# Kernel optimization log

Hardware: AMD Instinct MI355X
Metric: run time of the kernel (lower is better)

## Reference

```python
import jax, jax.numpy as jnp
import numpy as np

N = 50000          # num nodes
E = 800000         # num edges
NEG_SLOPE = 0.2    # leaky relu slope for attention logits


def gat_layer(h, W, al, ar, src, dst, res_W=None, res_identity=False, apply_elu=False):
    """One GATConv layer (DGL semantics, dropout=0, fc bias-free).
    h: [N, F_in]; W: [F_in, H*D]; al, ar: [H, D]. Returns [N, H, D]."""
    H, D = al.shape
    feat = (h @ W).reshape(N, H, D)                      # projected features
    el = jnp.sum(feat * al, axis=-1)                     # [N, H]
    er = jnp.sum(feat * ar, axis=-1)                     # [N, H]
    e = jax.nn.leaky_relu(el[src] + er[dst], NEG_SLOPE)  # [E, H] edge logits
    # numerically-stable edge softmax segmented over destination nodes
    m = jax.ops.segment_max(e, dst, num_segments=N)      # [N, H]
    m = jnp.where(jnp.isfinite(m), m, 0.0)               # nodes with no in-edges
    ex = jnp.exp(e - m[dst])
    den = jax.ops.segment_sum(ex, dst, num_segments=N)   # [N, H]
    alpha = ex / (den[dst] + 1e-9)                       # [E, H]
    # message passing: gather src feats, weight by alpha, scatter-add to dst
    out = jax.ops.segment_sum(feat[src] * alpha[..., None], dst, num_segments=N)
    if res_identity:
        out = out + h.reshape(N, H, D)
    elif res_W is not None:
        out = out + (h @ res_W).reshape(N, H, D)
    if apply_elu:
        out = jax.nn.elu(out)
    return out


def setup_inputs() -> dict:
    key = jax.random.key(0)
    ks = jax.random.split(key, 14)
    s = 0.1  # keep attention logits tame
    return {
        "features": jax.random.normal(ks[0], (N, 128), jnp.float32),
        "W0": jax.random.normal(ks[1], (128, 128), jnp.float32) * s,
        "al0": jax.random.normal(ks[2], (4, 32), jnp.float32) * s,
        "ar0": jax.random.normal(ks[3], (4, 32), jnp.float32) * s,
        "W1": jax.random.normal(ks[4], (128, 128), jnp.float32) * s,
        "al1": jax.random.normal(ks[5], (4, 32), jnp.float32) * s,
        "ar1": jax.random.normal(ks[6], (4, 32), jnp.float32) * s,
        "W2": jax.random.normal(ks[7], (128, 40), jnp.float32) * s,
        "al2": jax.random.normal(ks[8], (1, 40), jnp.float32) * s,
        "ar2": jax.random.normal(ks[9], (1, 40), jnp.float32) * s,
        "resW2": jax.random.normal(ks[10], (128, 40), jnp.float32) * s,
        "src": jax.random.randint(ks[11], (E,), 0, N, jnp.int32),
        "dst": jax.random.randint(ks[12], (E,), 0, N, jnp.int32),
    }


def reference(features, W0, al0, ar0, W1, al1, ar1, W2, al2, ar2, resW2, src, dst):
    # hidden layer 0: no residual, elu, flatten heads
    h = gat_layer(features, W0, al0, ar0, src, dst, apply_elu=True).reshape(N, -1)
    # hidden layer 1: residual (identity since in == heads*out), elu, flatten
    h = gat_layer(h, W1, al1, ar1, src, dst, res_identity=True, apply_elu=True).reshape(N, -1)
    # output layer: residual projection, no activation, mean over heads
    logits = gat_layer(h, W2, al2, ar2, src, dst, res_W=resW2).mean(axis=1)
    return logits
```

## Files before the change

kernel.cpp:

```cpp
#include <hip/hip_runtime.h>
#include <hip/hip_fp16.h>

#define NNODES 50000
#define NEDGES 800000

typedef _Float16 f16x8 __attribute__((ext_vector_type(8)));
typedef float f32x4 __attribute__((ext_vector_type(4)));

__global__ void k_count(const int* __restrict__ dst, int* __restrict__ cnt, int ne) {
  int e = blockIdx.x * 256 + threadIdx.x;
  if (e < ne) atomicAdd(&cnt[dst[e]], 1);
}

__global__ __launch_bounds__(1024) void k_blocksum(const int* __restrict__ cnt,
                                                   int* __restrict__ bsum, int n) {
  __shared__ int sb[1024];
  int t = threadIdx.x, i = blockIdx.x * 1024 + t;
  sb[t] = (i < n) ? cnt[i] : 0;
  __syncthreads();
  for (int m = 512; m; m >>= 1) {
    if (t < m) sb[t] += sb[t + m];
    __syncthreads();
  }
  if (t == 0) bsum[blockIdx.x] = sb[0];
}

__global__ void k_scanb(const int* __restrict__ bsum, int* __restrict__ bpre, int nb) {
  if (threadIdx.x == 0) {
    int s = 0;
    for (int i = 0; i < nb; ++i) { bpre[i] = s; s += bsum[i]; }
  }
}

__global__ __launch_bounds__(1024) void k_scanwrite(int* __restrict__ cnt,
                                                    const int* __restrict__ bpre,
                                                    int* __restrict__ row_off, int n) {
  __shared__ int sb[1024];
  int t = threadIdx.x, i = blockIdx.x * 1024 + t;
  int v = (i < n) ? cnt[i] : 0;
  sb[t] = v;
  __syncthreads();
  for (int off = 1; off < 1024; off <<= 1) {
    int x = (t >= off) ? sb[t - off] : 0;
    __syncthreads();
    sb[t] += x;
    __syncthreads();
  }
  int incl = sb[t] + bpre[blockIdx.x];
  if (i < n) {
    row_off[i + 1] = incl;
    cnt[i] = incl - v;
  }
  if (i == 0) row_off[0] = 0;
}

__global__ void k_fill(const int* __restrict__ src, const int* __restrict__ dst,
                       int* __restrict__ cursor, int* __restrict__ esrc, int ne) {
  int e = blockIdx.x * 256 + threadIdx.x;
  if (e < ne) {
    int pos = atomicAdd(&cursor[dst[e]], 1);
    esrc[pos] = src[e];
  }
}

__global__ __launch_bounds__(128) void k_prep(const float* __restrict__ W0, const float* __restrict__ al0,
                                              const float* __restrict__ ar0,
                                              const float* __restrict__ W1, const float* __restrict__ al1,
                                              const float* __restrict__ ar1,
                                              const float* __restrict__ W2, const float* __restrict__ resW2,
                                              const float* __restrict__ al2, const float* __restrict__ ar2,
                                              _Float16* __restrict__ Wt0, _Float16* __restrict__ Wt1,
                                              _Float16* __restrict__ Wt2) {
  int b = blockIdx.x, k = threadIdx.x;
  if (b < 288) {
    const float* W = (b < 144) ? W0 : W1;
    const float* al = (b < 144) ? al0 : al1;
    const float* ar = (b < 144) ? ar0 : ar1;
    _Float16* Wt = (b < 144) ? Wt0 : Wt1;
    int c = (b < 144) ? b : b - 144;
    float v = 0.f;
    if (c < 128) {
      v = W[k * 128 + c];
    } else if (c < 136) {
      int h = c - 128;
      const float* av = (h < 4) ? al : ar;
      int hh = h & 3;
      float s = 0.f;
      for (int d = 0; d < 32; ++d) s += W[k * 128 + hh * 32 + d] * av[hh * 32 + d];
      v = s;
    }
    Wt[c * 128 + k] = (_Float16)v;
  } else {
    int c = b - 288;
    float v = 0.f;
    if (c < 40) {
      v = W2[k * 40 + c];
    } else if (c < 80) {
      v = resW2[k * 40 + (c - 40)];
    } else if (c == 80) {
      float s = 0.f;
      for (int d = 0; d < 40; ++d) s += W2[k * 40 + d] * al2[d];
      v = s;
    } else if (c == 81) {
      float s = 0.f;
      for (int d = 0; d < 40; ++d) s += W2[k * 40 + d] * ar2[d];
      v = s;
    }
    Wt2[c * 128 + k] = (_Float16)v;
  }
}

template <int NCT, bool L2E>
__global__ __launch_bounds__(512) void k_gemm_mfma(const float* __restrict__ A,
                                                   const _Float16* __restrict__ Wtg,
                                                   __half* __restrict__ C,
                                                   float* __restrict__ resOut,
                                                   float* __restrict__ el,
                                                   float* __restrict__ er, int nrows) {
  __shared__ _Float16 Ah[128 * 136];
  __shared__ _Float16 Wl[NCT * 16 * 136];
  int t = threadIdx.x;
  int r0 = blockIdx.x * 128;

  for (int q = t; q < NCT * 16 * 16; q += 512) {
    int row = q >> 4, k8 = (q & 15) * 8;
    *(f16x8*)(&Wl[row * 136 + k8]) = *(const f16x8*)(Wtg + row * 128 + k8);
  }
  #pragma unroll
  for (int p = 0; p < 8; ++p) {
    int q = p * 512 + t;
    int r = q >> 5, k4 = (q & 31) * 4;
    float4 v = make_float4(0.f, 0.f, 0.f, 0.f);
    if (r0 + r < nrows) v = *(const float4*)(A + (size_t)(r0 + r) * 128 + k4);
    union { _Float16 h[4]; uint2 u; } pk;
    pk.h[0] = (_Float16)v.x; pk.h[1] = (_Float16)v.y;
    pk.h[2] = (_Float16)v.z; pk.h[3] = (_Float16)v.w;
    *(uint2*)(&Ah[r * 136 + k4]) = pk.u;
  }
  __syncthreads();

  int wave = t >> 6, l = t & 63;
  const _Float16* abase = &Ah[(wave * 16 + (l & 15)) * 136 + ((l >> 4) * 8)];
  const _Float16* bbase = &Wl[(l & 15) * 136 + ((l >> 4) * 8)];

  f32x4 acc[NCT] = {};
  #pragma unroll
  for (int ks = 0; ks < 4; ++ks) {
    f16x8 af = *(const f16x8*)(abase + ks * 32);
    #pragma unroll
    for (int nt = 0; nt < NCT; ++nt) {
      f16x8 bf = *(const f16x8*)(bbase + nt * 16 * 136 + ks * 32);
      acc[nt] = __builtin_amdgcn_mfma_f32_16x16x32_f16(af, bf, acc[nt], 0, 0, 0);
    }
  }

  int cc = l & 15;
  int rbase = r0 + wave * 16 + (l >> 4) * 4;
  #pragma unroll
  for (int r = 0; r < 4; ++r) {
    int row = rbase + r;
    if (row >= nrows) continue;
    if (!L2E) {
      #pragma unroll
      for (int nt = 0; nt < 8; ++nt)
        C[(size_t)row * 128 + nt * 16 + cc] = __float2half_rn(acc[nt][r]);
      float v = acc[8][r];
      if (cc < 4) el[row * 4 + cc] = v;
      else if (cc < 8) er[row * 4 + (cc - 4)] = v;
    } else {
      #pragma unroll
      for (int nt = 0; nt < 6; ++nt) {
        int col = nt * 16 + cc;
        float v = acc[nt][r];
        if (col < 40) C[(size_t)row * 40 + col] = __float2half_rn(v);
        else if (col < 80) resOut[(size_t)row * 40 + (col - 40)] = v;
        else if (col == 80) el[row] = v;
        else if (col == 81) er[row] = v;
      }
    }
  }
}

__device__ __forceinline__ void fma8h(float4& a0, float4& a1, float w, const uint4& r) {
  const __half2* hp = (const __half2*)&r;
  float2 f0 = __half22float2(hp[0]);
  float2 f1 = __half22float2(hp[1]);
  float2 f2 = __half22float2(hp[2]);
  float2 f3 = __half22float2(hp[3]);
  a0.x += w * f0.x; a0.y += w * f0.y; a0.z += w * f1.x; a0.w += w * f1.y;
  a1.x += w * f2.x; a1.y += w * f2.y; a1.z += w * f3.x; a1.w += w * f3.y;
}

template <bool RES, bool DOELU>
__global__ __launch_bounds__(256) void k_msg128v4(const __half* __restrict__ feat,
                                                  const float* __restrict__ el,
                                                  const float* __restrict__ er,
                                                  const int* __restrict__ row_off,
                                                  const int* __restrict__ esrc,
                                                  const float* __restrict__ hres,
                                                  float* __restrict__ out, int nnodes) {
  int t = threadIdx.x;
  int n = blockIdx.x * 16 + (t >> 4);
  if (n >= nnodes) return;
  int lane = t & 15;
  int h = lane >> 2;
  int s = row_off[n], e = row_off[n + 1];
  float ern = er[n * 4 + h];
  float4 acc0[4] = {}, acc1[4] = {};
  float den[4] = {0.f, 0.f, 0.f, 0.f};

  for (int c = s; c < e; c += 16) {
    int m = e - c; if (m > 16) m = 16;
    int sjv = 0;
    if (lane < m) sjv = esrc[c + lane];
    int e0 = __shfl(sjv, (lane & 3), 16);
    int e1 = __shfl(sjv, (lane & 3) + 4, 16);
    int e2 = __shfl(sjv, (lane & 3) + 8, 16);
    int e3 = __shfl(sjv, (lane & 3) + 12, 16);
    float sel0 = el[e0 * 4 + h];
    float sel1 = el[e1 * 4 + h];
    float sel2 = el[e2 * 4 + h];
    float sel3 = el[e3 * 4 + h];

#define GAT_SUB(KK, SEL)                                                      \
    {                                                                         \
      int b = KK * 4;                                                         \
      if (b < m) {                                                            \
        int mm = m - b; if (mm > 4) mm = 4;                                   \
        _Pragma("unroll")                                                     \
        for (int j = 0; j < 4; ++j) {                                         \
          if (j < mm) {                                                       \
            float ev = __shfl(SEL, (lane & 12) | j, 16);                      \
            float x = ev + ern;                                               \
            x = fmaxf(x, 0.2f * x);                                           \
            float wgt = __expf(x);                                            \
            int sj = __shfl(sjv, b + j, 16);                                  \
            den[j] += wgt;                                                    \
            uint4 raw = *(const uint4*)(feat + (size_t)sj * 128 + lane * 8);  \
            fma8h(acc0[j], acc1[j], wgt, raw);                                \
          }                                                                   \
        }                                                                     \
      }                                                                       \
    }
    GAT_SUB(0, sel0)
    GAT_SUB(1, sel1)
    GAT_SUB(2, sel2)
    GAT_SUB(3, sel3)
#undef GAT_SUB
  }

  float4 A0, A1;
  A0.x = (acc0[0].x + acc0[1].x) + (acc0[2].x + acc0[3].x);
  A0.y = (acc0[0].y + acc0[1].y) + (acc0[2].y + acc0[3].y);
  A0.z = (acc0[0].z + acc0[1].z) + (acc0[2].z + acc0[3].z);
  A0.w = (acc0[0].w + acc0[1].w) + (acc0[2].w + acc0[3].w);
  A1.x = (acc1[0].x + acc1[1].x) + (acc1[2].x + acc1[3].x);
  A1.y = (acc1[0].y + acc1[1].y) + (acc1[2].y + acc1[3].y);
  A1.z = (acc1[0].z + acc1[1].z) + (acc1[2].z + acc1[3].z);
  A1.w = (acc1[0].w + acc1[1].w) + (acc1[2].w + acc1[3].w);
  float D = (den[0] + den[1]) + (den[2] + den[3]);
  float inv = (e > s) ? 1.f / D : 0.f;
  A0.x *= inv; A0.y *= inv; A0.z *= inv; A0.w *= inv;
  A1.x *= inv; A1.y *= inv; A1.z *= inv; A1.w *= inv;
  if (RES) {
    float4 r0 = *(const float4*)(hres + (size_t)n * 128 + lane * 8);
    float4 r1 = *(const float4*)(hres + (size_t)n * 128 + lane * 8 + 4);
    A0.x += r0.x; A0.y += r0.y; A0.z += r0.z; A0.w += r0.w;
    A1.x += r1.x; A1.y += r1.y; A1.z += r1.z; A1.w += r1.w;
  }
  if (DOELU) {
    A0.x = (A0.x > 0.f) ? A0.x : expm1f(A0.x);
    A0.y = (A0.y > 0.f) ? A0.y : expm1f(A0.y);
    A0.z = (A0.z > 0.f) ? A0.z : expm1f(A0.z);
    A0.w = (A0.w > 0.f) ? A0.w : expm1f(A0.w);
    A1.x = (A1.x > 0.f) ? A1.x : expm1f(A1.x);
    A1.y = (A1.y > 0.f) ? A1.y : expm1f(A1.y);
    A1.z = (A1.z > 0.f) ? A1.z : expm1f(A1.z);
    A1.w = (A1.w > 0.f) ? A1.w : expm1f(A1.w);
  }
  *(float4*)(out + (size_t)n * 128 + lane * 8) = A0;
  *(float4*)(out + (size_t)n * 128 + lane * 8 + 4) = A1;
}

__global__ __launch_bounds__(256) void k_msg40v4(const __half* __restrict__ feat,
                                                 const float* __restrict__ el,
                                                 const float* __restrict__ er,
                                                 const int* __restrict__ row_off,
                                                 const int* __restrict__ esrc,
                                                 const float* __restrict__ res,
                                                 float* __restrict__ out, int nnodes) {
  int t = threadIdx.x;
  int n = blockIdx.x * 16 + (t >> 4);
  if (n >= nnodes) return;
  int lane = t & 15;
  int s = row_off[n], e = row_off[n + 1];
  float ern = er[n];
  float4 acc[2] = {};
  float den[2] = {0.f, 0.f};

  for (int c = s; c < e; c += 16) {
    int m = e - c; if (m > 16) m = 16;
    int sjv = 0;
    if (lane < m) sjv = esrc[c + lane];
    float selv = el[sjv];
    #pragma unroll
    for (int j = 0; j < 16; ++j) {
      if (j < m) {
        float ev = __shfl(selv, j, 16);
        float x = ev + ern;
        x = fmaxf(x, 0.2f * x);
        float wgt = __expf(x);
        int sj = __shfl(sjv, j, 16);
        den[j & 1] += wgt;
        if (lane < 10) {
          uint2 raw = *(const uint2*)(feat + (size_t)sj * 40 + lane * 4);
          const __half2* hp = (const __half2*)&raw;
          float2 f0 = __half22float2(hp[0]);
          float2 f1 = __half22float2(hp[1]);
          acc[j & 1].x += wgt * f0.x;
          acc[j & 1].y += wgt * f0.y;
          acc[j & 1].z += wgt * f1.x;
          acc[j & 1].w += wgt * f1.y;
        }
      }
    }
  }
  float D = den[0] + den[1];
  float inv = (e > s) ? 1.f / D : 0.f;
  if (lane < 10) {
    float4 r = *(const float4*)(res + (size_t)n * 40 + lane * 4);
    float4 A;
    A.x = (acc[0].x + acc[1].x) * inv + r.x;
    A.y = (acc[0].y + acc[1].y) * inv + r.y;
    A.z = (acc[0].z + acc[1].z) * inv + r.z;
    A.w = (acc[0].w + acc[1].w) * inv + r.w;
    *(float4*)(out + (size_t)n * 40 + lane * 4) = A;
  }
}

extern "C" void kernel_launch(void* const* d_in, const int* in_sizes, int n_in,
                              void* d_out, int out_size, void* d_ws, size_t ws_size,
                              hipStream_t stream) {
  const float* features = (const float*)d_in[0];
  const float* W0 = (const float*)d_in[1];
  const float* al0 = (const float*)d_in[2];
  const float* ar0 = (const float*)d_in[3];
  const float* W1 = (const float*)d_in[4];
  const float* al1 = (const float*)d_in[5];
  const float* ar1 = (const float*)d_in[6];
  const float* W2 = (const float*)d_in[7];
  const float* al2 = (const float*)d_in[8];
  const float* ar2 = (const float*)d_in[9];
  const float* resW2 = (const float*)d_in[10];
  const int* src = (const int*)d_in[11];
  const int* dst = (const int*)d_in[12];
  float* out = (float*)d_out;

  const int N = NNODES, E = NEDGES;
  char* w = (char*)d_ws;
  auto alloc = [&](size_t bytes) {
    char* p = w;
    w += (bytes + 255) & ~(size_t)255;
    return p;
  };
  int* cnt = (int*)alloc((size_t)N * 4);
  int* row_off = (int*)alloc((size_t)(N + 1) * 4);
  int* bsum = (int*)alloc(256 * 4);
  int* bpre = (int*)alloc(256 * 4);
  int* esrc = (int*)alloc((size_t)E * 4);
  __half* feath = (__half*)alloc((size_t)N * 128 * 2);
  float* res2 = (float*)alloc((size_t)N * 40 * 4);
  float* el = (float*)alloc((size_t)N * 4 * 4);
  float* er = (float*)alloc((size_t)N * 4 * 4);
  float* h1 = (float*)alloc((size_t)N * 128 * 4);
  float* h2 = (float*)alloc((size_t)N * 128 * 4);
  _Float16* Wt0 = (_Float16*)alloc(144 * 128 * 2);
  _Float16* Wt1 = (_Float16*)alloc(144 * 128 * 2);
  _Float16* Wt2 = (_Float16*)alloc(96 * 128 * 2);
  __half* feat2h = feath;

  const int NB = (N + 1023) / 1024;

  k_prep<<<384, 128, 0, stream>>>(W0, al0, ar0, W1, al1, ar1, W2, resW2, al2, ar2,
                                  Wt0, Wt1, Wt2);

  hipMemsetAsync(cnt, 0, (size_t)N * 4, stream);
  k_count<<<(E + 255) / 256, 256, 0, stream>>>(dst, cnt, E);
  k_blocksum<<<NB, 1024, 0, stream>>>(cnt, bsum, N);
  k_scanb<<<1, 64, 0, stream>>>(bsum, bpre, NB);
  k_scanwrite<<<NB, 1024, 0, stream>>>(cnt, bpre, row_off, N);
  k_fill<<<(E + 255) / 256, 256, 0, stream>>>(src, dst, cnt, esrc, E);

  const int GB128 = (N + 127) / 128;
  const int GM = (N + 15) / 16;

  k_gemm_mfma<9, false><<<GB128, 512, 0, stream>>>(features, Wt0, feath, nullptr, el, er, N);
  k_msg128v4<false, true><<<GM, 256, 0, stream>>>(feath, el, er, row_off, esrc, nullptr, h1, N);

  k_gemm_mfma<9, false><<<GB128, 512, 0, stream>>>(h1, Wt1, feath, nullptr, el, er, N);
  k_msg128v4<true, true><<<GM, 256, 0, stream>>>(feath, el, er, row_off, esrc, h1, h2, N);

  k_gemm_mfma<6, true><<<GB128, 512, 0, stream>>>(h2, Wt2, feat2h, res2, el, er, N);
  k_msg40v4<<<GM, 256, 0, stream>>>(feat2h, el, er, row_off, esrc, res2, out, N);
}
```

Before: 252.0 us.

## Replace atomic CSR build with two-level bucket sort using LDS atomics

Replaces the global-atomic count/scan/fill CSR construction with a packed (dst<<16|src) key, a per-slice bucket histogram over 1024-node buckets, and a stable ballot-based compaction into buckets. A per-bucket LDS counting sort then writes row offsets and source indices. The aim is to remove heavy global atomic contention and the scattered atomic fill. In exchange it adds extra passes over the edge array, and the k_compact grid rescans its whole slice once per bucket.

```diff
diff --git a/kernel.cpp b/kernel.cpp
--- a/kernel.cpp
+++ b/kernel.cpp
@@ -3,41 +3,40 @@
 
 #define NNODES 50000
 #define NEDGES 800000
+#define NBUCK 49
+#define NSLICE 16
+#define SLICE_E 50000
+#define CHUNK_E 3125
 
 typedef _Float16 f16x8 __attribute__((ext_vector_type(8)));
 typedef float f32x4 __attribute__((ext_vector_type(4)));
 
-__global__ void k_count(const int* __restrict__ dst, int* __restrict__ cnt, int ne) {
-  int e = blockIdx.x * 256 + threadIdx.x;
-  if (e < ne) atomicAdd(&cnt[dst[e]], 1);
-}
-
-__global__ __launch_bounds__(1024) void k_blocksum(const int* __restrict__ cnt,
-                                                   int* __restrict__ bsum, int n) {
+
+__global__ __launch_bounds__(256) void k_packhist(const int* __restrict__ src,
+                                                  const int* __restrict__ dst,
+                                                  unsigned* __restrict__ pack,
+                                                  int* __restrict__ hist2) {
+  __shared__ int h[NBUCK];
+  int t = threadIdx.x, j = blockIdx.x;
+  int s = j >> 4, c = j & 15;
+  if (t < NBUCK) h[t] = 0;
+  __syncthreads();
+  int beg = s * SLICE_E + c * CHUNK_E;
+  for (int q = t; q < CHUNK_E; q += 256) {
+    int e = beg + q;
+    unsigned d = (unsigned)dst[e], sv = (unsigned)src[e];
+    pack[e] = (d << 16) | sv;
+    atomicAdd(&h[d >> 10], 1);
+  }
+  __syncthreads();
+  if (t < NBUCK) atomicAdd(&hist2[t * NSLICE + s], h[t]);
+}
+
+__global__ __launch_bounds__(1024) void k_scan784(const int* __restrict__ hist2,
+                                                  int* __restrict__ off2) {
   __shared__ int sb[1024];
-  int t = threadIdx.x, i = blockIdx.x * 1024 + t;
-  sb[t] = (i < n) ? cnt[i] : 0;
-  __syncthreads();
-  for (int m = 512; m; m >>= 1) {
-    if (t < m) sb[t] += sb[t + m];
-    __syncthreads();
-  }
-  if (t == 0) bsum[blockIdx.x] = sb[0];
-}
-
-__global__ void k_scanb(const int* __restrict__ bsum, int* __restrict__ bpre, int nb) {
-  if (threadIdx.x == 0) {
-    int s = 0;
-    for (int i = 0; i < nb; ++i) { bpre[i] = s; s += bsum[i]; }
-  }
-}
-
-__global__ __launch_bounds__(1024) void k_scanwrite(int* __restrict__ cnt,
-                                                    const int* __restrict__ bpre,
-                                                    int* __restrict__ row_off, int n) {
-  __shared__ int sb[1024];
-  int t = threadIdx.x, i = blockIdx.x * 1024 + t;
-  int v = (i < n) ? cnt[i] : 0;
+  int t = threadIdx.x;
+  int v = (t < NBUCK * NSLICE) ? hist2[t] : 0;
   sb[t] = v;
   __syncthreads();
   for (int off = 1; off < 1024; off <<= 1) {
@@ -46,20 +45,78 @@
     sb[t] += x;
     __syncthreads();
   }
-  int incl = sb[t] + bpre[blockIdx.x];
-  if (i < n) {
-    row_off[i + 1] = incl;
-    cnt[i] = incl - v;
-  }
-  if (i == 0) row_off[0] = 0;
-}
-
-__global__ void k_fill(const int* __restrict__ src, const int* __restrict__ dst,
-                       int* __restrict__ cursor, int* __restrict__ esrc, int ne) {
-  int e = blockIdx.x * 256 + threadIdx.x;
-  if (e < ne) {
-    int pos = atomicAdd(&cursor[dst[e]], 1);
-    esrc[pos] = src[e];
+  if (t < NBUCK * NSLICE) off2[t] = sb[t] - v;
+}
+
+__global__ __launch_bounds__(1024) void k_compact(const unsigned* __restrict__ pack,
+                                                  const int* __restrict__ off2,
+                                                  unsigned* __restrict__ bucketed) {
+  __shared__ int lw[16];
+  int t = threadIdx.x, j = blockIdx.x;
+  int b = j >> 4, s = j & 15;
+  int wbase = off2[b * NSLICE + s];
+  int beg = s * SLICE_E, end = beg + SLICE_E;
+  int wid = t >> 6, lane = t & 63;
+  for (int i0 = beg; i0 < end; i0 += 1024) {
+    int i = i0 + t;
+    unsigned v = 0;
+    bool match = false;
+    if (i < end) {
+      v = pack[i];
+      match = ((int)(v >> 26) == b);
+    }
+    unsigned long long mb = __ballot(match);
+    if (lane == 0) lw[wid] = __popcll(mb);
+    __syncthreads();
+    int wex = 0, tot = 0;
+    #pragma unroll
+    for (int k = 0; k < 16; ++k) {
+      int cc = lw[k];
+      if (k < wid) wex += cc;
+      tot += cc;
+    }
+    if (match) {
+      int rank = wex + __popcll(mb & ((1ull << lane) - 1ull));
+      bucketed[wbase + rank] = v;
+    }
+    wbase += tot;
+    __syncthreads();
+  }
+}
+
+__global__ __launch_bounds__(1024) void k_sortbkt(const unsigned* __restrict__ bucketed,
+                                                  const int* __restrict__ off2,
+                                                  int* __restrict__ row_off,
+                                                  int* __restrict__ esrc) {
+  __shared__ int cnt[1024];
+  __shared__ int cur[1024];
+  int t = threadIdx.x, b = blockIdx.x;
+  int base = off2[b * NSLICE];
+  int endb = (b == NBUCK - 1) ? NEDGES : off2[(b + 1) * NSLICE];
+  int ne = endb - base;
+  cnt[t] = 0;
+  __syncthreads();
+  for (int i = t; i < ne; i += 1024)
+    atomicAdd(&cnt[(bucketed[base + i] >> 16) & 1023], 1);
+  __syncthreads();
+  int orig = cnt[t];
+  cur[t] = orig;
+  __syncthreads();
+  for (int off = 1; off < 1024; off <<= 1) {
+    int x = (t >= off) ? cur[t - off] : 0;
+    __syncthreads();
+    cur[t] += x;
+    __syncthreads();
+  }
+  int excl = cur[t] - orig;
+  int g = (b << 10) + t;
+  if (g <= NNODES) row_off[g] = base + excl;
+  cur[t] = excl;
+  __syncthreads();
+  for (int i = t; i < ne; i += 1024) {
+    unsigned v = bucketed[base + i];
+    int pos = base + atomicAdd(&cur[(v >> 16) & 1023], 1);
+    esrc[pos] = (int)(v & 0xFFFFu);
   }
 }
 
@@ -356,18 +413,19 @@
   const int* dst = (const int*)d_in[12];
   float* out = (float*)d_out;
 
-  const int N = NNODES, E = NEDGES;
+  const int N = NNODES;
   char* w = (char*)d_ws;
   auto alloc = [&](size_t bytes) {
     char* p = w;
     w += (bytes + 255) & ~(size_t)255;
     return p;
   };
-  int* cnt = (int*)alloc((size_t)N * 4);
   int* row_off = (int*)alloc((size_t)(N + 1) * 4);
-  int* bsum = (int*)alloc(256 * 4);
-  int* bpre = (int*)alloc(256 * 4);
-  int* esrc = (int*)alloc((size_t)E * 4);
+  int* esrc = (int*)alloc((size_t)NEDGES * 4);
+  unsigned* pack = (unsigned*)alloc((size_t)NEDGES * 4);
+  unsigned* bucketed = (unsigned*)alloc((size_t)NEDGES * 4);
+  int* hist2 = (int*)alloc(NBUCK * NSLICE * 4);
+  int* off2 = (int*)alloc(NBUCK * NSLICE * 4);
   __half* feath = (__half*)alloc((size_t)N * 128 * 2);
   float* res2 = (float*)alloc((size_t)N * 40 * 4);
   float* el = (float*)alloc((size_t)N * 4 * 4);
@@ -379,17 +437,14 @@
   _Float16* Wt2 = (_Float16*)alloc(96 * 128 * 2);
   __half* feat2h = feath;
 
-  const int NB = (N + 1023) / 1024;
-
   k_prep<<<384, 128, 0, stream>>>(W0, al0, ar0, W1, al1, ar1, W2, resW2, al2, ar2,
                                   Wt0, Wt1, Wt2);
 
-  hipMemsetAsync(cnt, 0, (size_t)N * 4, stream);
-  k_count<<<(E + 255) / 256, 256, 0, stream>>>(dst, cnt, E);
-  k_blocksum<<<NB, 1024, 0, stream>>>(cnt, bsum, N);
-  k_scanb<<<1, 64, 0, stream>>>(bsum, bpre, NB);
-  k_scanwrite<<<NB, 1024, 0, stream>>>(cnt, bpre, row_off, N);
-  k_fill<<<(E + 255) / 256, 256, 0, stream>>>(src, dst, cnt, esrc, E);
+  hipMemsetAsync(hist2, 0, NBUCK * NSLICE * 4, stream);
+  k_packhist<<<256, 256, 0, stream>>>(src, dst, pack, hist2);
+  k_scan784<<<1, 1024, 0, stream>>>(hist2, off2);
+  k_compact<<<NBUCK * NSLICE, 1024, 0, stream>>>(pack, off2, bucketed);
+  k_sortbkt<<<NBUCK, 1024, 0, stream>>>(bucketed, off2, row_off, esrc);
 
   const int GB128 = (N + 127) / 128;
   const int GM = (N + 15) / 16;
```

Result: slower. 263.1 us (+4.4%).
